# Kernel optimization log

Hardware: AMD Instinct MI355X
Metric: run time of the kernel (lower is better)

## Reference

```python
import jax, jax.numpy as jnp
import numpy as np

N_NODES = 50000


def setup_inputs() -> dict:
    key = jax.random.key(0)
    k1, k2, k3, k4 = jax.random.split(key, 4)
    x = jax.random.normal(k1, (N_NODES, 128), dtype=jnp.float32)
    edge_index = jax.random.randint(k2, (2, 800000), 0, N_NODES, dtype=jnp.int64)
    W = jax.random.normal(k3, (128, 128), dtype=jnp.float32) * 0.05
    b = jax.random.normal(k4, (128,), dtype=jnp.float32) * 0.05
    return {"x": x, "edge_index": edge_index, "W": W, "b": b}


def reference(x, edge_index, W, b):
    # x: [N, C_in], edge_index: [2, E]
    row, col = edge_index[0], edge_index[1]
    n = x.shape[0]
    # degree of each node as a source (bincount over row)
    deg = jax.ops.segment_sum(jnp.ones_like(row, dtype=x.dtype), row, num_segments=n)
    # deg^{-1/2} with inf -> 0 (deg == 0 case)
    deg_inv_sqrt = jnp.where(deg > 0, jax.lax.rsqrt(jnp.maximum(deg, 1.0)) * jnp.where(deg > 0, 1.0, 0.0), 0.0)
    deg_inv_sqrt = jnp.where(deg > 0, deg ** -0.5, 0.0)
    norm = deg_inv_sqrt[row] * deg_inv_sqrt[col]  # [E]
    # gather, scale, scatter-add: agg[row] += x[col] * norm
    msgs = x[col] * norm[:, None]  # [E, C_in]
    agg = jax.ops.segment_sum(msgs, row, num_segments=n)  # [N, C_in]
    # linear
    return agg @ W.T + b
```

## Files before the change

### kernel.cpp

```cpp
#include <hip/hip_runtime.h>
#include <hip/hip_bf16.h>


typedef short v8s __attribute__((ext_vector_type(8)));
typedef float v4f __attribute__((ext_vector_type(4)));

#define ELLCAP 64
#define BINCAP 4608
#define ROWSTRIDE 136

static __device__ __forceinline__ unsigned int f2bf(float f) {
    __hip_bfloat16 h = __float2bfloat16(f);
    return (unsigned int)__builtin_bit_cast(unsigned short, h);
}

__global__ __launch_bounds__(256) void k_binA(
    const int* __restrict__ idx, int* __restrict__ gbin,
    unsigned int* __restrict__ pairs, const float4* __restrict__ w4,
    ushort4* __restrict__ wb4, int E, int nbins) {
    int b = blockIdx.x;
    const int t = threadIdx.x;
    if (b < 16) {
        int i = b * 256 + t;
        float4 v = w4[i];
        ushort4 o;
        o.x = (unsigned short)f2bf(v.x);
        o.y = (unsigned short)f2bf(v.y);
        o.z = (unsigned short)f2bf(v.z);
        o.w = (unsigned short)f2bf(v.w);
        wb4[i] = o;
        return;
    }
    b -= 16;
    __shared__ int hist[256];
    __shared__ int base[256];
    hist[t] = 0;
    __syncthreads();

    int e0 = b * 2048 + t * 8;
    int nv = E - e0;
    nv = nv > 8 ? 8 : (nv < 0 ? 0 : nv);
    int rows[8], cols[8];
    if (nv == 8) {
        int4 a0 = *(const int4*)&idx[e0];
        int4 a1 = *(const int4*)&idx[e0 + 4];
        int4 c0 = *(const int4*)&idx[E + e0];
        int4 c1 = *(const int4*)&idx[E + e0 + 4];
        rows[0] = a0.x; rows[1] = a0.y; rows[2] = a0.z; rows[3] = a0.w;
        rows[4] = a1.x; rows[5] = a1.y; rows[6] = a1.z; rows[7] = a1.w;
        cols[0] = c0.x; cols[1] = c0.y; cols[2] = c0.z; cols[3] = c0.w;
        cols[4] = c1.x; cols[5] = c1.y; cols[6] = c1.z; cols[7] = c1.w;
    } else {
        for (int k = 0; k < 8; ++k) {
            rows[k] = (k < nv) ? idx[e0 + k] : 0;
            cols[k] = (k < nv) ? idx[E + e0 + k] : 0;
        }
    }
#pragma unroll
    for (int k = 0; k < 8; ++k)
        if (k < nv) atomicAdd(&hist[rows[k] >> 8], 1);
    __syncthreads();
    if (t < nbins) base[t] = atomicAdd(&gbin[t], hist[t]);
    __syncthreads();
    hist[t] = 0;
    __syncthreads();
#pragma unroll
    for (int k = 0; k < 8; ++k) {
        if (k < nv) {
            int bin = rows[k] >> 8;
            int pos = base[bin] + atomicAdd(&hist[bin], 1);
            if (pos < BINCAP)
                pairs[(size_t)bin * BINCAP + pos] =
                    (unsigned)(((rows[k] & 255) << 16) | cols[k]);
        }
    }
}

__global__ __launch_bounds__(1024) void k_binB(
    const unsigned int* __restrict__ pairs, const int* __restrict__ gbin,
    unsigned short* __restrict__ ell, unsigned char* __restrict__ degc,
    float* __restrict__ dis, const float2* __restrict__ x2,
    unsigned int* __restrict__ xs32, int N) {
    __shared__ __align__(16) unsigned short lell[256 * ELLCAP];
    __shared__ int cnt_l[256];
    __shared__ float sdis[256];
    const int bin = blockIdx.x;
    const int t = threadIdx.x;
    if (t < 256) cnt_l[t] = 0;
    __syncthreads();

    int m = gbin[bin];
    if (m > BINCAP) m = BINCAP;
    for (int i = t; i < m; i += 1024) {
        unsigned pv = pairs[(size_t)bin * BINCAP + i];
        int local = pv >> 16;
        int slot = atomicAdd(&cnt_l[local], 1);
        if (slot < ELLCAP) lell[local * ELLCAP + slot] = (unsigned short)(pv & 0xFFFF);
    }
    __syncthreads();

    if (t < 256) {
        int r = bin * 256 + t;
        float s = 0.f;
        if (r < N) {
            int d = cnt_l[t];
            s = (d > 0) ? rsqrtf((float)d) : 0.0f;
            dis[r] = s;
            degc[r] = (unsigned char)(d > ELLCAP ? ELLCAP : d);
        }
        sdis[t] = s;
    }
    __syncthreads();

    {
        unsigned int* gell = (unsigned int*)(ell + (size_t)bin * 256 * ELLCAP);
        const unsigned int* sell = (const unsigned int*)lell;
        for (int i = t; i < 8192; i += 1024) gell[i] = sell[i];
    }

    size_t xbase = (size_t)bin * 16384;
    for (int i = t; i < 16384; i += 1024) {
        int lr = i >> 6;
        unsigned ov = 0u;
        if (bin * 256 + lr < N) {
            float2 v = x2[xbase + i];
            float ss = sdis[lr];
            ov = f2bf(v.x * ss) | (f2bf(v.y * ss) << 16);
        }
        xs32[xbase + i] = ov;
    }
}

__global__ __launch_bounds__(256) void k_fused(
    const unsigned short* __restrict__ ell, const unsigned char* __restrict__ degc,
    const float* __restrict__ dis, const unsigned int* __restrict__ xs32,
    const v8s* __restrict__ Wb8, const float* __restrict__ bias,
    float* __restrict__ out, int N) {
    __shared__ __align__(16) unsigned short smem[32 * ROWSTRIDE];
    const int nb0 = blockIdx.x * 32;
    const int wv = threadIdx.x >> 6, lane = threadIdx.x & 63;

    for (int i = 0; i < 8; ++i) {
        int lrow = wv * 8 + i;
        int n = nb0 + lrow;
        float acc0 = 0.f, acc1 = 0.f;
        if (n < N) {
            int d = degc[n];
            int cl = ell[(size_t)n * ELLCAP + lane];
            int c = (lane < d) ? cl : N;
            for (int j = 0; j < d; j += 16) {
                int cc[16];
#pragma unroll
                for (int u = 0; u < 16; ++u)
                    cc[u] = __builtin_amdgcn_readlane(c, j + u);
                unsigned uu[16];
#pragma unroll
                for (int u = 0; u < 16; ++u)
                    uu[u] = xs32[(size_t)cc[u] * 64 + lane];
#pragma unroll
                for (int u = 0; u < 16; ++u) {
                    acc0 += __builtin_bit_cast(float, uu[u] << 16);
                    acc1 += __builtin_bit_cast(float, uu[u] & 0xFFFF0000u);
                }
            }
            float s = dis[n];
            acc0 *= s;
            acc1 *= s;
        }
        unsigned pack = f2bf(acc0) | (f2bf(acc1) << 16);
        *(unsigned int*)&smem[(size_t)lrow * ROWSTRIDE + lane * 2] = pack;
    }
    __syncthreads();

    {
        int quad = lane >> 4, m16 = lane & 15;
        int lrow = (wv & 1) * 16 + m16;
        v8s afrag[4];
#pragma unroll
        for (int kk = 0; kk < 4; ++kk)
            afrag[kk] = *(const v8s*)&smem[lrow * ROWSTRIDE + kk * 32 + quad * 8];
        int rbase = nb0 + (wv & 1) * 16 + quad * 4;
        int jbase = (wv >> 1) * 64;
#pragma unroll
        for (int jt = 0; jt < 4; ++jt) {
            int jcol = jbase + jt * 16 + m16;
            v4f acc = {0.f, 0.f, 0.f, 0.f};
#pragma unroll
            for (int kk = 0; kk < 4; ++kk) {
                v8s bfrag = Wb8[jcol * 16 + kk * 4 + quad];
                acc = __builtin_amdgcn_mfma_f32_16x16x32_bf16(afrag[kk], bfrag,
                                                              acc, 0, 0, 0);
            }
            float bj = bias[jcol];
#pragma unroll
            for (int r = 0; r < 4; ++r) {
                int row = rbase + r;
                if (row < N) out[(size_t)row * 128 + jcol] = acc[r] + bj;
            }
        }
    }
}

extern "C" void kernel_launch(void* const* d_in, const int* in_sizes, int n_in,
                              void* d_out, int out_size, void* d_ws, size_t ws_size,
                              hipStream_t stream) {
    const float* x = (const float*)d_in[0];
    const int* idx = (const int*)d_in[1];
    const float* W = (const float*)d_in[2];
    const float* b = (const float*)d_in[3];
    float* out = (float*)d_out;

    const int N = in_sizes[0] / 128;
    const int E = in_sizes[1] / 2;
    const int nbins = (N + 255) / 256;
    const int nrows = nbins * 256;

    char* p = (char*)d_ws;
    auto alloc = [&](size_t bytes) {
        char* r = p;
        p += (bytes + 63) & ~(size_t)63;
        return r;
    };
    int* gbin = (int*)alloc((size_t)nbins * 4);
    unsigned short* ell = (unsigned short*)alloc((size_t)nrows * ELLCAP * 2);
    unsigned int* pairs = (unsigned int*)alloc((size_t)nbins * BINCAP * 4);
    float* dis = (float*)alloc((size_t)N * 4);
    unsigned char* degc = (unsigned char*)alloc((size_t)N);
    unsigned int* xs = (unsigned int*)alloc((size_t)nrows * 128 * 2);
    ushort4* wb = (ushort4*)alloc(128 * 128 * 2);

    hipMemsetAsync(gbin, 0, (size_t)nbins * sizeof(int), stream);

    const int ablocks = 16 + (E + 2047) / 2048;
    k_binA<<<ablocks, 256, 0, stream>>>(idx, gbin, pairs, (const float4*)W, wb, E,
                                        nbins);
    k_binB<<<nbins, 1024, 0, stream>>>(pairs, gbin, ell, degc, dis,
                                       (const float2*)x, xs, N);
    k_fused<<<(N + 31) / 32, 256, 0, stream>>>(ell, degc, dis, xs, (const v8s*)wb,
                                               b, out, N);
}
```

Baseline: 150.0 us.

## Move x bf16 conversion into binning kernel and apply source norm during gather

The x-to-bf16 conversion no longer waits for degrees. It now runs in extra blocks of the first binning kernel, alongside the edge histogram work, and no longer pre-scales rows by the source's deg^-1/2. The aggregation kernel instead loads dis[col] per neighbour and folds it in with an fma. Padding slots index N, so dis gets one extra zero entry. This shortens the serial second kernel and overlaps the conversion traffic with binning, at the cost of 16 extra scalar gathers per chunk in the hot loop.

```diff
diff --git a/kernel.cpp b/kernel.cpp
--- a/kernel.cpp
+++ b/kernel.cpp
@@ -17,10 +17,13 @@
 __global__ __launch_bounds__(256) void k_binA(
     const int* __restrict__ idx, int* __restrict__ gbin,
     unsigned int* __restrict__ pairs, const float4* __restrict__ w4,
-    ushort4* __restrict__ wb4, int E, int nbins) {
+    ushort4* __restrict__ wb4, const float2* __restrict__ x2,
+    unsigned int* __restrict__ xs32, float* __restrict__ dis,
+    int E, int nbins, int N) {
     int b = blockIdx.x;
     const int t = threadIdx.x;
     if (b < 16) {
+        if (b == 0 && t == 0) dis[N] = 0.f;
         int i = b * 256 + t;
         float4 v = w4[i];
         ushort4 o;
@@ -32,6 +35,21 @@
         return;
     }
     b -= 16;
+    if (b < nbins) {
+        size_t xbase = (size_t)b * 16384;
+        int rbase = b * 256;
+        for (int i = t; i < 16384; i += 256) {
+            int lr = i >> 6;
+            unsigned ov = 0u;
+            if (rbase + lr < N) {
+                float2 v = x2[xbase + i];
+                ov = f2bf(v.x) | (f2bf(v.y) << 16);
+            }
+            xs32[xbase + i] = ov;
+        }
+        return;
+    }
+    b -= nbins;
     __shared__ int hist[256];
     __shared__ int base[256];
     hist[t] = 0;
@@ -79,11 +97,9 @@
 __global__ __launch_bounds__(1024) void k_binB(
     const unsigned int* __restrict__ pairs, const int* __restrict__ gbin,
     unsigned short* __restrict__ ell, unsigned char* __restrict__ degc,
-    float* __restrict__ dis, const float2* __restrict__ x2,
-    unsigned int* __restrict__ xs32, int N) {
+    float* __restrict__ dis, int N) {
     __shared__ __align__(16) unsigned short lell[256 * ELLCAP];
     __shared__ int cnt_l[256];
-    __shared__ float sdis[256];
     const int bin = blockIdx.x;
     const int t = threadIdx.x;
     if (t < 256) cnt_l[t] = 0;
@@ -101,14 +117,14 @@
 
     if (t < 256) {
         int r = bin * 256 + t;
-        float s = 0.f;
         if (r < N) {
             int d = cnt_l[t];
-            s = (d > 0) ? rsqrtf((float)d) : 0.0f;
+            float s = (d > 0) ? rsqrtf((float)d) : 0.0f;
             dis[r] = s;
             degc[r] = (unsigned char)(d > ELLCAP ? ELLCAP : d);
-        }
-        sdis[t] = s;
+        } else if (r == N) {
+            dis[N] = 0.f;
+        }
     }
     __syncthreads();
 
@@ -116,18 +132,6 @@
         unsigned int* gell = (unsigned int*)(ell + (size_t)bin * 256 * ELLCAP);
         const unsigned int* sell = (const unsigned int*)lell;
         for (int i = t; i < 8192; i += 1024) gell[i] = sell[i];
-    }
-
-    size_t xbase = (size_t)bin * 16384;
-    for (int i = t; i < 16384; i += 1024) {
-        int lr = i >> 6;
-        unsigned ov = 0u;
-        if (bin * 256 + lr < N) {
-            float2 v = x2[xbase + i];
-            float ss = sdis[lr];
-            ov = f2bf(v.x * ss) | (f2bf(v.y * ss) << 16);
-        }
-        xs32[xbase + i] = ov;
     }
 }
 
@@ -157,10 +161,14 @@
 #pragma unroll
                 for (int u = 0; u < 16; ++u)
                     uu[u] = xs32[(size_t)cc[u] * 64 + lane];
+                float dcv[16];
+#pragma unroll
+                for (int u = 0; u < 16; ++u)
+                    dcv[u] = dis[cc[u]];
 #pragma unroll
                 for (int u = 0; u < 16; ++u) {
-                    acc0 += __builtin_bit_cast(float, uu[u] << 16);
-                    acc1 += __builtin_bit_cast(float, uu[u] & 0xFFFF0000u);
+                    acc0 = fmaf(dcv[u], __builtin_bit_cast(float, uu[u] << 16), acc0);
+                    acc1 = fmaf(dcv[u], __builtin_bit_cast(float, uu[u] & 0xFFFF0000u), acc1);
                 }
             }
             float s = dis[n];
@@ -224,18 +232,17 @@
     int* gbin = (int*)alloc((size_t)nbins * 4);
     unsigned short* ell = (unsigned short*)alloc((size_t)nrows * ELLCAP * 2);
     unsigned int* pairs = (unsigned int*)alloc((size_t)nbins * BINCAP * 4);
-    float* dis = (float*)alloc((size_t)N * 4);
+    float* dis = (float*)alloc((size_t)(N + 1) * 4);
     unsigned char* degc = (unsigned char*)alloc((size_t)N);
     unsigned int* xs = (unsigned int*)alloc((size_t)nrows * 128 * 2);
     ushort4* wb = (ushort4*)alloc(128 * 128 * 2);
 
     hipMemsetAsync(gbin, 0, (size_t)nbins * sizeof(int), stream);
 
-    const int ablocks = 16 + (E + 2047) / 2048;
-    k_binA<<<ablocks, 256, 0, stream>>>(idx, gbin, pairs, (const float4*)W, wb, E,
-                                        nbins);
-    k_binB<<<nbins, 1024, 0, stream>>>(pairs, gbin, ell, degc, dis,
-                                       (const float2*)x, xs, N);
+    const int ablocks = 16 + nbins + (E + 2047) / 2048;
+    k_binA<<<ablocks, 256, 0, stream>>>(idx, gbin, pairs, (const float4*)W, wb,
+                                        (const float2*)x, xs, dis, E, nbins, N);
+    k_binB<<<nbins, 1024, 0, stream>>>(pairs, gbin, ell, degc, dis, N);
     k_fused<<<(N + 31) / 32, 256, 0, stream>>>(ell, degc, dis, xs, (const v8s*)wb,
                                                b, out, N);
 }
```

Measured after the change: 175.1 us. 16.7% more time.
